# Performance work log

Measured on AMD Instinct MI355X. Metric: run time of the kernel, lower is better.

Reference implementation:

```python
import jax, jax.numpy as jnp
import numpy as np

D_MODEL = 768
N_HEAD = 12
D_HEAD = D_MODEL // N_HEAD
B, T = 2, 2048


def setup_inputs() -> dict:
    key = jax.random.key(0)
    k1, k2, k3 = jax.random.split(key, 3)
    x = jax.random.normal(k1, (B, T, D_MODEL), dtype=jnp.float32)
    w_attn = jax.random.normal(k2, (D_MODEL, 3 * D_MODEL), dtype=jnp.float32) * (1.0 / np.sqrt(D_MODEL))
    b_attn = jnp.zeros((3 * D_MODEL,), dtype=jnp.float32)
    w_proj = jax.random.normal(k3, (D_MODEL, D_MODEL), dtype=jnp.float32) * (1.0 / np.sqrt(D_MODEL))
    b_proj = jnp.zeros((D_MODEL,), dtype=jnp.float32)
    return {"x": x, "w_attn": w_attn, "b_attn": b_attn, "w_proj": w_proj, "b_proj": b_proj}


def reference(x, w_attn, b_attn, w_proj, b_proj):
    Bq, Tq, C = x.shape
    qkv = x @ w_attn + b_attn                                  # [B, T, 3C]
    qkv = qkv.reshape(Bq, Tq, 3, N_HEAD, D_HEAD)
    q, k, v = qkv[:, :, 0], qkv[:, :, 1], qkv[:, :, 2]         # [B, T, H, Dh]
    scale = 1.0 / np.sqrt(D_HEAD)
    att = jnp.einsum('bqhd,bkhd->bhqk', q, k) * scale          # [B, H, T, T]
    causal = jnp.tril(jnp.ones((Tq, Tq), dtype=bool))
    att = jnp.where(causal[None, None], att, -jnp.inf)
    att = jax.nn.softmax(att, axis=-1)
    y = jnp.einsum('bhqk,bkhd->bqhd', att, v).reshape(Bq, Tq, C)
    return y @ w_proj + b_proj
```

## Files before the change

kernel.cpp:

```cpp
#include <hip/hip_runtime.h>
#include <hip/hip_bf16.h>

#define D_MODEL 768
#define N_HEADS 12
#define D_HEADK 64
#define BB 2
#define TT 2048
#define M_TOK (BB*TT)
#define N_QKV (3*D_MODEL)

using f32x4 = __attribute__((ext_vector_type(4))) float;
using s16x8 = __attribute__((ext_vector_type(8))) short;

__device__ __forceinline__ float fast_exp2(float x) {
    return __builtin_amdgcn_exp2f(x);
}

__device__ __forceinline__ unsigned short f2bf(float f) {
    union { float f; unsigned u; } v; v.f = f;
    unsigned r = v.u + 0x7FFFu + ((v.u >> 16) & 1u);
    return (unsigned short)(r >> 16);
}

__global__ void xbf_kernel(const float* __restrict__ X, unsigned short* __restrict__ Xb) {
    int idx = (blockIdx.x * 256 + threadIdx.x) * 8;
    float4 v0 = *(const float4*)&X[idx];
    float4 v1 = *(const float4*)&X[idx + 4];
    ushort4 u0, u1;
    u0.x = f2bf(v0.x); u0.y = f2bf(v0.y); u0.z = f2bf(v0.z); u0.w = f2bf(v0.w);
    u1.x = f2bf(v1.x); u1.y = f2bf(v1.y); u1.z = f2bf(v1.z); u1.w = f2bf(v1.w);
    *(ushort4*)&Xb[idx]     = u0;
    *(ushort4*)&Xb[idx + 4] = u1;
}

__global__ void wtrans_kernel(const float* __restrict__ Wa, const float* __restrict__ Wp,
                              unsigned short* __restrict__ Wta, unsigned short* __restrict__ Wtp) {
    const float* W; unsigned short* Wt; int N;
    if (blockIdx.z == 0) { W = Wa; Wt = Wta; N = N_QKV; }
    else                 { W = Wp; Wt = Wtp; N = D_MODEL; }
    int bx = blockIdx.x * 32;
    if (bx >= N) return;
    int by = blockIdx.y * 32;
    __shared__ float tile[32][33];
    int tx = threadIdx.x & 31;
    int ty = threadIdx.x >> 5;
    #pragma unroll
    for (int i = ty; i < 32; i += 8)
        tile[i][tx] = W[(size_t)(by + i) * N + bx + tx];
    __syncthreads();
    #pragma unroll
    for (int i = ty; i < 32; i += 8)
        Wt[(size_t)(bx + i) * D_MODEL + by + tx] = f2bf(tile[tx][i]);
}

__launch_bounds__(256)
__global__ void qkv_kernel(const unsigned short* __restrict__ Xb, const unsigned short* __restrict__ Wt,
                           const float* __restrict__ bias,
                           unsigned short* __restrict__ Qw, unsigned short* __restrict__ Kw,
                           unsigned short* __restrict__ Vw) {
    __shared__ unsigned short As[128][40];
    __shared__ unsigned short Bs[128][40];
    const int m0 = blockIdx.y * 128;
    const int n0 = blockIdx.x * 128;
    const int tid = threadIdx.x;
    const int l  = tid & 63;
    const int w  = tid >> 6;
    const int wr = w >> 1, wc = w & 1;
    const int lr = l & 15, lk = (l >> 4) * 8, li = (l >> 4) * 4;

    f32x4 acc[4][4] = {};
    for (int kt = 0; kt < D_MODEL; kt += 32) {
        #pragma unroll
        for (int p = 0; p < 2; ++p) {
            int ch = tid * 2 + p;
            int r = ch >> 2;
            int c = (ch & 3) * 8;
            *(int4*)&As[r][c] = *(const int4*)&Xb[(size_t)(m0 + r) * D_MODEL + kt + c];
            *(int4*)&Bs[r][c] = *(const int4*)&Wt[(size_t)(n0 + r) * D_MODEL + kt + c];
        }
        __syncthreads();
        s16x8 a[4], bf[4];
        #pragma unroll
        for (int mi = 0; mi < 4; ++mi)
            a[mi] = *(const s16x8*)&As[wr*64 + mi*16 + lr][lk];
        #pragma unroll
        for (int ni = 0; ni < 4; ++ni)
            bf[ni] = *(const s16x8*)&Bs[wc*64 + ni*16 + lr][lk];
        #pragma unroll
        for (int mi = 0; mi < 4; ++mi)
            #pragma unroll
            for (int ni = 0; ni < 4; ++ni)
                acc[mi][ni] = __builtin_amdgcn_mfma_f32_16x16x32_bf16(a[mi], bf[ni], acc[mi][ni], 0, 0, 0);
        __syncthreads();
    }
    #pragma unroll
    for (int ni = 0; ni < 4; ++ni) {
        int ng = n0 + wc*64 + ni*16 + lr;
        int mat = ng / D_MODEL;
        int hd  = ng % D_MODEL;
        int h = hd >> 6, d = hd & 63;
        float bv = bias[ng];
        #pragma unroll
        for (int mi = 0; mi < 4; ++mi) {
            #pragma unroll
            for (int i = 0; i < 4; ++i) {
                int t  = m0 + wr*64 + mi*16 + li + i;
                int b  = t >> 11, tq = t & 2047;
                float val = acc[mi][ni][i] + bv;
                size_t off = ((size_t)(b*N_HEADS + h)*TT + tq)*64 + d;
                if (mat == 0)      Qw[off] = f2bf(val * 0.18033688f);
                else if (mat == 1) Kw[off] = f2bf(val);
                else               Vw[off] = f2bf(val);
            }
        }
    }
}

__launch_bounds__(256)
__global__ void vtrans_kernel(const unsigned short* __restrict__ Vw, unsigned short* __restrict__ Vt) {
    __shared__ unsigned short tile[64][65];
    const int bh = blockIdx.y;
    const int t0 = blockIdx.x * 64;
    const int tid = threadIdx.x;
    const int srow = tid >> 3;
    const int scol = (tid & 7) * 8;
    const unsigned short* src = Vw + (size_t)bh * TT * 64;
    unsigned short* dst = Vt + (size_t)bh * 64 * TT;
    *(int4*)&tile[srow][scol]    = *(const int4*)&src[(size_t)(t0 + srow) * 64 + scol];
    *(int4*)&tile[srow+32][scol] = *(const int4*)&src[(size_t)(t0 + srow + 32) * 64 + scol];
    __syncthreads();
    s16x8 a0, a1;
    #pragma unroll
    for (int j = 0; j < 8; ++j) {
        a0[j] = (short)tile[scol + j][srow];
        a1[j] = (short)tile[scol + j][srow + 32];
    }
    *(s16x8*)&dst[(size_t)srow * TT + t0 + scol]        = a0;
    *(s16x8*)&dst[(size_t)(srow + 32) * TT + t0 + scol] = a1;
}

__launch_bounds__(256)
__global__ void attn_kernel(const unsigned short* __restrict__ Q,
                            const unsigned short* __restrict__ Kk,
                            const unsigned short* __restrict__ Vt,
                            unsigned short* __restrict__ Y) {
    __shared__ unsigned short Ks[64][72];
    __shared__ unsigned short Vs[64][72];
    __shared__ unsigned short Ps[4][16][72];
    const int bh = blockIdx.y;
    const int qb = gridDim.x - 1 - blockIdx.x;
    const int q0 = qb * 64;
    const int b = bh / N_HEADS, h = bh % N_HEADS;
    const int tid = threadIdx.x;
    const int l  = tid & 63;
    const int w  = tid >> 6;
    const int lr = l & 15, lg = l >> 4;
    const int lk = lg * 8, li = lg * 4;
    const int srow = tid >> 3;
    const int scol = (tid & 7) * 8;

    const unsigned short* Qp = Q  + (size_t)bh * TT * 64;
    const unsigned short* Kp = Kk + (size_t)bh * TT * 64;
    const unsigned short* Vp = Vt + (size_t)bh * 64 * TT;

    const int qw0 = q0 + w * 16;
    const s16x8 qa0 = *(const s16x8*)&Qp[(qw0 + lr)*64 + lk];
    const s16x8 qa1 = *(const s16x8*)&Qp[(qw0 + lr)*64 + lk + 32];

    float mi[4], si[4];
    f32x4 o[4] = {};
    #pragma unroll
    for (int i = 0; i < 4; ++i) { mi[i] = -1e30f; si[i] = 0.f; }

    const int niter = qb + 1;
    int4 kp0 = *(const int4*)&Kp[(size_t)srow * 64 + scol];
    int4 kp1 = *(const int4*)&Kp[(size_t)(srow + 32) * 64 + scol];
    int4 vp0 = *(const int4*)&Vp[(size_t)srow * TT + scol];
    int4 vp1 = *(const int4*)&Vp[(size_t)(srow + 32) * TT + scol];

    for (int it = 0; it < niter; ++it) {
        const int kt = it * 64;
        __syncthreads();
        *(int4*)&Ks[srow][scol]      = kp0;
        *(int4*)&Ks[srow + 32][scol] = kp1;
        *(int4*)&Vs[srow][scol]      = vp0;
        *(int4*)&Vs[srow + 32][scol] = vp1;
        __syncthreads();
        if (it + 1 < niter) {
            const int k2 = kt + 64;
            kp0 = *(const int4*)&Kp[(size_t)(k2 + srow) * 64 + scol];
            kp1 = *(const int4*)&Kp[(size_t)(k2 + srow + 32) * 64 + scol];
            vp0 = *(const int4*)&Vp[(size_t)srow * TT + k2 + scol];
            vp1 = *(const int4*)&Vp[(size_t)(srow + 32) * TT + k2 + scol];
        }
        f32x4 sc[4];
        #pragma unroll
        for (int kb = 0; kb < 4; ++kb) {
            s16x8 k0 = *(const s16x8*)&Ks[kb*16 + lr][lk];
            s16x8 k1 = *(const s16x8*)&Ks[kb*16 + lr][lk + 32];
            f32x4 z = {};
            z = __builtin_amdgcn_mfma_f32_16x16x32_bf16(qa0, k0, z, 0, 0, 0);
            z = __builtin_amdgcn_mfma_f32_16x16x32_bf16(qa1, k1, z, 0, 0, 0);
            sc[kb] = z;
        }
        if (kt + 63 > qw0) {
            #pragma unroll
            for (int kb = 0; kb < 4; ++kb) {
                int k = kt + kb*16 + lr;
                #pragma unroll
                for (int i = 0; i < 4; ++i)
                    if (k > qw0 + li + i) sc[kb][i] = -1e30f;
            }
        }
        #pragma unroll
        for (int i = 0; i < 4; ++i) {
            float lm = fmaxf(fmaxf(sc[0][i], sc[1][i]), fmaxf(sc[2][i], sc[3][i]));
            if (!__all(lm <= mi[i] + 11.5f)) {
                float pm = lm;
                #pragma unroll
                for (int off = 1; off < 16; off <<= 1)
                    pm = fmaxf(pm, __shfl_xor(pm, off, 64));
                float mn = fmaxf(mi[i], pm);
                float sf = fast_exp2(mi[i] - mn);
                si[i] *= sf;
                #pragma unroll
                for (int c = 0; c < 4; ++c) o[c][i] *= sf;
                mi[i] = mn;
            }
            float e0 = fast_exp2(sc[0][i] - mi[i]);
            float e1 = fast_exp2(sc[1][i] - mi[i]);
            float e2 = fast_exp2(sc[2][i] - mi[i]);
            float e3 = fast_exp2(sc[3][i] - mi[i]);
            si[i] += (e0 + e1) + (e2 + e3);
            Ps[w][li + i][lr]      = f2bf(e0);
            Ps[w][li + i][16 + lr] = f2bf(e1);
            Ps[w][li + i][32 + lr] = f2bf(e2);
            Ps[w][li + i][48 + lr] = f2bf(e3);
        }
        __builtin_amdgcn_wave_barrier();
        const s16x8 pa0 = *(const s16x8*)&Ps[w][lr][lk];
        const s16x8 pa1 = *(const s16x8*)&Ps[w][lr][lk + 32];
        #pragma unroll
        for (int c = 0; c < 4; ++c) {
            s16x8 vb0 = *(const s16x8*)&Vs[c*16 + lr][lk];
            s16x8 vb1 = *(const s16x8*)&Vs[c*16 + lr][lk + 32];
            o[c] = __builtin_amdgcn_mfma_f32_16x16x32_bf16(pa0, vb0, o[c], 0, 0, 0);
            o[c] = __builtin_amdgcn_mfma_f32_16x16x32_bf16(pa1, vb1, o[c], 0, 0, 0);
        }
    }
    #pragma unroll
    for (int i = 0; i < 4; ++i) {
        float s = si[i];
        #pragma unroll
        for (int off = 1; off < 16; off <<= 1)
            s += __shfl_xor(s, off, 64);
        float inv = 1.f / s;
        int t = b*TT + q0 + w*16 + li + i;
        #pragma unroll
        for (int c = 0; c < 4; ++c)
            Y[(size_t)t*D_MODEL + h*64 + c*16 + lr] = f2bf(o[c][i] * inv);
    }
}

__launch_bounds__(256)
__global__ void proj_kernel(const unsigned short* __restrict__ Y, const unsigned short* __restrict__ Wt,
                            const float* __restrict__ bias, float* __restrict__ Out) {
    __shared__ unsigned short As[128][40];
    __shared__ unsigned short Bs[128][40];
    const int m0 = blockIdx.y * 128;
    const int n0 = blockIdx.x * 128;
    const int tid = threadIdx.x;
    const int l  = tid & 63;
    const int w  = tid >> 6;
    const int wr = w >> 1, wc = w & 1;
    const int lr = l & 15, lk = (l >> 4) * 8, li = (l >> 4) * 4;

    f32x4 acc[4][4] = {};
    for (int kt = 0; kt < D_MODEL; kt += 32) {
        #pragma unroll
        for (int p = 0; p < 2; ++p) {
            int ch = tid * 2 + p;
            int r = ch >> 2;
            int c = (ch & 3) * 8;
            *(int4*)&As[r][c] = *(const int4*)&Y[(size_t)(m0 + r) * D_MODEL + kt + c];
            *(int4*)&Bs[r][c] = *(const int4*)&Wt[(size_t)(n0 + r) * D_MODEL + kt + c];
        }
        __syncthreads();
        s16x8 a[4], bf[4];
        #pragma unroll
        for (int mi = 0; mi < 4; ++mi)
            a[mi] = *(const s16x8*)&As[wr*64 + mi*16 + lr][lk];
        #pragma unroll
        for (int ni = 0; ni < 4; ++ni)
            bf[ni] = *(const s16x8*)&Bs[wc*64 + ni*16 + lr][lk];
        #pragma unroll
        for (int mi = 0; mi < 4; ++mi)
            #pragma unroll
            for (int ni = 0; ni < 4; ++ni)
                acc[mi][ni] = __builtin_amdgcn_mfma_f32_16x16x32_bf16(a[mi], bf[ni], acc[mi][ni], 0, 0, 0);
        __syncthreads();
    }
    #pragma unroll
    for (int ni = 0; ni < 4; ++ni) {
        int ng = n0 + wc*64 + ni*16 + lr;
        float bv = bias[ng];
        #pragma unroll
        for (int mj = 0; mj < 4; ++mj)
            #pragma unroll
            for (int i = 0; i < 4; ++i) {
                int t = m0 + wr*64 + mj*16 + li + i;
                Out[(size_t)t*D_MODEL + ng] = acc[mj][ni][i] + bv;
            }
    }
}

extern "C" void kernel_launch(void* const* d_in, const int* in_sizes, int n_in,
                              void* d_out, int out_size, void* d_ws, size_t ws_size,
                              hipStream_t stream) {
    const float* x      = (const float*)d_in[0];
    const float* w_attn = (const float*)d_in[1];
    const float* b_attn = (const float*)d_in[2];
    const float* w_proj = (const float*)d_in[3];
    const float* b_proj = (const float*)d_in[4];
    float* out = (float*)d_out;

    unsigned short* wt_attn = (unsigned short*)d_ws;
    unsigned short* wt_proj = wt_attn + (size_t)N_QKV * D_MODEL;
    unsigned short* Qw      = wt_proj + (size_t)D_MODEL * D_MODEL;
    unsigned short* Kw      = Qw + (size_t)M_TOK * D_MODEL;
    unsigned short* Vw      = Kw + (size_t)M_TOK * D_MODEL;
    unsigned short* Yw      = Vw + (size_t)M_TOK * D_MODEL;
    unsigned short* Xb      = Yw + (size_t)M_TOK * D_MODEL;
    unsigned short* Vtw     = Xb;

    hipLaunchKernelGGL(xbf_kernel, dim3(M_TOK*D_MODEL/2048), dim3(256), 0, stream, x, Xb);
    hipLaunchKernelGGL(wtrans_kernel, dim3(N_QKV/32, D_MODEL/32, 2), dim3(256), 0, stream,
                       w_attn, w_proj, wt_attn, wt_proj);
    hipLaunchKernelGGL(qkv_kernel, dim3(N_QKV/128, M_TOK/128), dim3(256), 0, stream,
                       Xb, wt_attn, b_attn, Qw, Kw, Vw);
    hipLaunchKernelGGL(vtrans_kernel, dim3(TT/64, BB*N_HEADS), dim3(256), 0, stream,
                       Vw, Vtw);
    hipLaunchKernelGGL(attn_kernel, dim3(TT/64, BB*N_HEADS), dim3(256), 0, stream,
                       Qw, Kw, Vtw, Yw);
    hipLaunchKernelGGL(proj_kernel, dim3(D_MODEL/128, M_TOK/128), dim3(256), 0, stream,
                       Yw, wt_proj, b_proj, out);
}
```

Measured before the change: 201.5 us.

## Rewrite attention with 32x32 MFMA, register-resident P, and swizzled LDS

Reworks the attention kernel so each wave handles 32 query rows using 32x32x16 bf16 MFMA with S computed transposed (K as A operand). P stays in registers via packed bf16 conversion and permlane32 swaps instead of a round-trip through shared memory. The 64x72 padded tiles are replaced by XOR-swizzled 64x64 LDS tiles, and each block now covers 128 queries, halving the grid. Fully masked 32-key subtiles are skipped. The costs are more register pressure, fewer blocks in flight, and more per-row shuffles when the online-softmax rescale runs.

```diff
diff --git a/kernel.cpp b/kernel.cpp
--- a/kernel.cpp
+++ b/kernel.cpp
@@ -9,8 +9,9 @@
 #define M_TOK (BB*TT)
 #define N_QKV (3*D_MODEL)
 
-using f32x4 = __attribute__((ext_vector_type(4))) float;
-using s16x8 = __attribute__((ext_vector_type(8))) short;
+using f32x4  = __attribute__((ext_vector_type(4))) float;
+using f32x16 = __attribute__((ext_vector_type(16))) float;
+using s16x8  = __attribute__((ext_vector_type(8))) short;
 
 __device__ __forceinline__ float fast_exp2(float x) {
     return __builtin_amdgcn_exp2f(x);
@@ -20,6 +21,12 @@
     union { float f; unsigned u; } v; v.f = f;
     unsigned r = v.u + 0x7FFFu + ((v.u >> 16) & 1u);
     return (unsigned short)(r >> 16);
+}
+
+__device__ __forceinline__ unsigned cvtpk_bf16(float lo, float hi) {
+    unsigned d;
+    asm("v_cvt_pk_bf16_f32 %0, %1, %2" : "=v"(d) : "v"(lo), "v"(hi));
+    return d;
 }
 
 __global__ void xbf_kernel(const float* __restrict__ X, unsigned short* __restrict__ Xb) {
@@ -139,40 +146,47 @@
     *(s16x8*)&dst[(size_t)(srow + 32) * TT + t0 + scol] = a1;
 }
 
+__device__ __forceinline__ int swz(int r, int c) { return r*64 + (c ^ ((r & 7) << 3)); }
+
 __launch_bounds__(256)
 __global__ void attn_kernel(const unsigned short* __restrict__ Q,
                             const unsigned short* __restrict__ Kk,
                             const unsigned short* __restrict__ Vt,
                             unsigned short* __restrict__ Y) {
-    __shared__ unsigned short Ks[64][72];
-    __shared__ unsigned short Vs[64][72];
-    __shared__ unsigned short Ps[4][16][72];
+    __shared__ unsigned short Ks[64*64];
+    __shared__ unsigned short Vs[64*64];
     const int bh = blockIdx.y;
     const int qb = gridDim.x - 1 - blockIdx.x;
-    const int q0 = qb * 64;
+    const int q0 = qb * 128;
     const int b = bh / N_HEADS, h = bh % N_HEADS;
     const int tid = threadIdx.x;
     const int l  = tid & 63;
     const int w  = tid >> 6;
-    const int lr = l & 15, lg = l >> 4;
-    const int lk = lg * 8, li = lg * 4;
+    const int lq = l & 31;
+    const int hi = l >> 5;
     const int srow = tid >> 3;
     const int scol = (tid & 7) * 8;
+    const int qw0 = q0 + w * 32;
 
     const unsigned short* Qp = Q  + (size_t)bh * TT * 64;
     const unsigned short* Kp = Kk + (size_t)bh * TT * 64;
     const unsigned short* Vp = Vt + (size_t)bh * 64 * TT;
 
-    const int qw0 = q0 + w * 16;
-    const s16x8 qa0 = *(const s16x8*)&Qp[(qw0 + lr)*64 + lk];
-    const s16x8 qa1 = *(const s16x8*)&Qp[(qw0 + lr)*64 + lk + 32];
-
-    float mi[4], si[4];
-    f32x4 o[4] = {};
-    #pragma unroll
-    for (int i = 0; i < 4; ++i) { mi[i] = -1e30f; si[i] = 0.f; }
-
-    const int niter = qb + 1;
+    s16x8 qsel[4];
+    {
+        const unsigned short* qrow = &Qp[(size_t)(qw0 + lq) * 64];
+        #pragma unroll
+        for (int t = 0; t < 4; ++t) {
+            s16x8 qlo = *(const s16x8*)&qrow[16*t];
+            s16x8 qhi = *(const s16x8*)&qrow[16*t + 8];
+            qsel[t] = hi ? qhi : qlo;
+        }
+    }
+
+    float mi = -1e30f, si = 0.f;
+    f32x16 o0 = {}, o1 = {};
+
+    const int niter = 2 * (qb + 1);
     int4 kp0 = *(const int4*)&Kp[(size_t)srow * 64 + scol];
     int4 kp1 = *(const int4*)&Kp[(size_t)(srow + 32) * 64 + scol];
     int4 vp0 = *(const int4*)&Vp[(size_t)srow * TT + scol];
@@ -181,10 +195,10 @@
     for (int it = 0; it < niter; ++it) {
         const int kt = it * 64;
         __syncthreads();
-        *(int4*)&Ks[srow][scol]      = kp0;
-        *(int4*)&Ks[srow + 32][scol] = kp1;
-        *(int4*)&Vs[srow][scol]      = vp0;
-        *(int4*)&Vs[srow + 32][scol] = vp1;
+        *(int4*)&Ks[swz(srow,      scol)] = kp0;
+        *(int4*)&Ks[swz(srow + 32, scol)] = kp1;
+        *(int4*)&Vs[swz(srow,      scol)] = vp0;
+        *(int4*)&Vs[swz(srow + 32, scol)] = vp1;
         __syncthreads();
         if (it + 1 < niter) {
             const int k2 = kt + 64;
@@ -193,72 +207,75 @@
             vp0 = *(const int4*)&Vp[(size_t)srow * TT + k2 + scol];
             vp1 = *(const int4*)&Vp[(size_t)(srow + 32) * TT + k2 + scol];
         }
-        f32x4 sc[4];
-        #pragma unroll
-        for (int kb = 0; kb < 4; ++kb) {
-            s16x8 k0 = *(const s16x8*)&Ks[kb*16 + lr][lk];
-            s16x8 k1 = *(const s16x8*)&Ks[kb*16 + lr][lk + 32];
-            f32x4 z = {};
-            z = __builtin_amdgcn_mfma_f32_16x16x32_bf16(qa0, k0, z, 0, 0, 0);
-            z = __builtin_amdgcn_mfma_f32_16x16x32_bf16(qa1, k1, z, 0, 0, 0);
-            sc[kb] = z;
-        }
-        if (kt + 63 > qw0) {
-            #pragma unroll
-            for (int kb = 0; kb < 4; ++kb) {
-                int k = kt + kb*16 + lr;
+        #pragma unroll
+        for (int kti = 0; kti < 2; ++kti) {
+            const int kk = kt + kti * 32;
+            if (kk > qw0) continue;
+            const bool diag = (kk == qw0);
+            f32x16 s = {};
+            #pragma unroll
+            for (int t = 0; t < 4; ++t) {
+                s16x8 a = *(const s16x8*)&Ks[swz(kti*32 + lq, 16*t + 8*hi)];
+                s = __builtin_amdgcn_mfma_f32_32x32x16_bf16(a, qsel[t], s, 0, 0, 0);
+            }
+            if (diag) {
                 #pragma unroll
-                for (int i = 0; i < 4; ++i)
-                    if (k > qw0 + li + i) sc[kb][i] = -1e30f;
-            }
-        }
-        #pragma unroll
-        for (int i = 0; i < 4; ++i) {
-            float lm = fmaxf(fmaxf(sc[0][i], sc[1][i]), fmaxf(sc[2][i], sc[3][i]));
-            if (!__all(lm <= mi[i] + 11.5f)) {
-                float pm = lm;
+                for (int r = 0; r < 16; ++r) {
+                    const int kloc = (r & 3) + 8*(r >> 2) + 4*hi;
+                    if (kloc > lq) s[r] = -1e30f;
+                }
+            }
+            float lm = s[0];
+            #pragma unroll
+            for (int r = 1; r < 16; ++r) lm = fmaxf(lm, s[r]);
+            if (!__all(lm <= mi + 11.5f)) {
+                float pm = fmaxf(lm, __shfl_xor(lm, 32));
+                float mn = fmaxf(mi, pm);
+                float sf = fast_exp2(mi - mn);
+                si *= sf;
                 #pragma unroll
-                for (int off = 1; off < 16; off <<= 1)
-                    pm = fmaxf(pm, __shfl_xor(pm, off, 64));
-                float mn = fmaxf(mi[i], pm);
-                float sf = fast_exp2(mi[i] - mn);
-                si[i] *= sf;
-                #pragma unroll
-                for (int c = 0; c < 4; ++c) o[c][i] *= sf;
-                mi[i] = mn;
-            }
-            float e0 = fast_exp2(sc[0][i] - mi[i]);
-            float e1 = fast_exp2(sc[1][i] - mi[i]);
-            float e2 = fast_exp2(sc[2][i] - mi[i]);
-            float e3 = fast_exp2(sc[3][i] - mi[i]);
-            si[i] += (e0 + e1) + (e2 + e3);
-            Ps[w][li + i][lr]      = f2bf(e0);
-            Ps[w][li + i][16 + lr] = f2bf(e1);
-            Ps[w][li + i][32 + lr] = f2bf(e2);
-            Ps[w][li + i][48 + lr] = f2bf(e3);
-        }
-        __builtin_amdgcn_wave_barrier();
-        const s16x8 pa0 = *(const s16x8*)&Ps[w][lr][lk];
-        const s16x8 pa1 = *(const s16x8*)&Ps[w][lr][lk + 32];
-        #pragma unroll
-        for (int c = 0; c < 4; ++c) {
-            s16x8 vb0 = *(const s16x8*)&Vs[c*16 + lr][lk];
-            s16x8 vb1 = *(const s16x8*)&Vs[c*16 + lr][lk + 32];
-            o[c] = __builtin_amdgcn_mfma_f32_16x16x32_bf16(pa0, vb0, o[c], 0, 0, 0);
-            o[c] = __builtin_amdgcn_mfma_f32_16x16x32_bf16(pa1, vb1, o[c], 0, 0, 0);
-        }
-    }
-    #pragma unroll
-    for (int i = 0; i < 4; ++i) {
-        float s = si[i];
-        #pragma unroll
-        for (int off = 1; off < 16; off <<= 1)
-            s += __shfl_xor(s, off, 64);
-        float inv = 1.f / s;
-        int t = b*TT + q0 + w*16 + li + i;
-        #pragma unroll
-        for (int c = 0; c < 4; ++c)
-            Y[(size_t)t*D_MODEL + h*64 + c*16 + lr] = f2bf(o[c][i] * inv);
+                for (int r = 0; r < 16; ++r) {
+                    const int qloc = (r & 3) + 8*(r >> 2) + 4*hi;
+                    float sfq = __shfl(sf, qloc);
+                    o0[r] *= sfq; o1[r] *= sfq;
+                }
+                mi = mn;
+            }
+            float e[16];
+            float psum = 0.f;
+            #pragma unroll
+            for (int r = 0; r < 16; ++r) {
+                e[r] = fast_exp2(s[r] - mi);
+                psum += e[r];
+            }
+            si += psum;
+            #pragma unroll
+            for (int s2 = 0; s2 < 2; ++s2) {
+                unsigned c0 = cvtpk_bf16(e[8*s2 + 0], e[8*s2 + 1]);
+                unsigned c1 = cvtpk_bf16(e[8*s2 + 2], e[8*s2 + 3]);
+                unsigned c2 = cvtpk_bf16(e[8*s2 + 4], e[8*s2 + 5]);
+                unsigned c3 = cvtpk_bf16(e[8*s2 + 6], e[8*s2 + 7]);
+                asm("v_permlane32_swap_b32 %0, %1" : "+v"(c0), "+v"(c2));
+                asm("v_permlane32_swap_b32 %0, %1" : "+v"(c1), "+v"(c3));
+                union { unsigned u[4]; s16x8 v; } pa;
+                pa.u[0] = c0; pa.u[1] = c1; pa.u[2] = c2; pa.u[3] = c3;
+                const int kc = kti*32 + 16*s2 + 8*hi;
+                s16x8 vb0 = *(const s16x8*)&Vs[swz(lq,      kc)];
+                s16x8 vb1 = *(const s16x8*)&Vs[swz(32 + lq, kc)];
+                o0 = __builtin_amdgcn_mfma_f32_32x32x16_bf16(pa.v, vb0, o0, 0, 0, 0);
+                o1 = __builtin_amdgcn_mfma_f32_32x32x16_bf16(pa.v, vb1, o1, 0, 0, 0);
+            }
+        }
+    }
+    float sfull = si + __shfl_xor(si, 32);
+    float invf = 1.f / sfull;
+    #pragma unroll
+    for (int r = 0; r < 16; ++r) {
+        const int qloc = (r & 3) + 8*(r >> 2) + 4*hi;
+        float iv = __shfl(invf, qloc);
+        size_t row = (size_t)(b*TT + qw0 + qloc) * D_MODEL + h*64;
+        Y[row + lq]      = f2bf(o0[r] * iv);
+        Y[row + 32 + lq] = f2bf(o1[r] * iv);
     }
 }
 
@@ -340,7 +357,7 @@
                        Xb, wt_attn, b_attn, Qw, Kw, Vw);
     hipLaunchKernelGGL(vtrans_kernel, dim3(TT/64, BB*N_HEADS), dim3(256), 0, stream,
                        Vw, Vtw);
-    hipLaunchKernelGGL(attn_kernel, dim3(TT/64, BB*N_HEADS), dim3(256), 0, stream,
+    hipLaunchKernelGGL(attn_kernel, dim3(TT/128, BB*N_HEADS), dim3(256), 0, stream,
                        Qw, Kw, Vtw, Yw);
     hipLaunchKernelGGL(proj_kernel, dim3(D_MODEL/128, M_TOK/128), dim3(256), 0, stream,
                        Yw, wt_proj, b_proj, out);
```

Measured after the change: 200.5 us. Within noise of the previous version (-0.5%).
